# Optimization experiments

Hardware: AMD Instinct MI355X
Metric: run time of the kernel (lower is better)

The kernel has to match this reference:

```python
import jax, jax.numpy as jnp
import numpy as np

B, S, FEAT, H, DK, MAX_ITEMS = 8, 1024, 512, 8, 64, 200
LN_EPS = 1e-5
NEG = -999999999.0


def _build_mask(seq_len):
    # rows before T = S-(maxItems+1) cannot see the tail block [T:];
    # tail rows T..S-2 cannot see columns >= their own index (strict upper wedge).
    T = seq_len - (MAX_ITEMS + 1)
    i = jnp.arange(seq_len)[:, None]
    j = jnp.arange(seq_len)[None, :]
    blocked = ((i < T) & (j >= T)) | ((i >= T) & (i <= seq_len - 2) & (j >= i))
    return jnp.where(blocked, NEG, 0.0).astype(jnp.float32)  # [S, S]


def setup_inputs() -> dict:
    key = jax.random.key(0)
    ks = jax.random.split(key, 6)
    def init(k, shape, fan_in):
        return (jax.random.normal(k, shape, jnp.float32) / np.sqrt(fan_in)).astype(jnp.float32)
    return {
        "x": jax.random.normal(ks[0], (B, S, FEAT), jnp.float32),
        "ln_gamma": jnp.ones((FEAT,), jnp.float32),
        "ln_beta": jnp.zeros((FEAT,), jnp.float32),
        "WQ": init(ks[1], (H, FEAT, DK), FEAT), "bq": jnp.zeros((H, DK), jnp.float32),
        "WK": init(ks[2], (H, FEAT, DK), FEAT), "bk": jnp.zeros((H, DK), jnp.float32),
        "WV": init(ks[3], (H, FEAT, DK), FEAT), "bv": jnp.zeros((H, DK), jnp.float32),
        "WO": init(ks[4], (H * DK, FEAT), H * DK), "bO": jnp.zeros((FEAT,), jnp.float32),
    }


def reference(x, ln_gamma, ln_beta, WQ, bq, WK, bk, WV, bv, WO, bO):
    b, s, f = x.shape
    # Pre-LN
    mu = jnp.mean(x, axis=-1, keepdims=True)
    var = jnp.mean((x - mu) ** 2, axis=-1, keepdims=True)
    xn = (x - mu) / jnp.sqrt(var + LN_EPS) * ln_gamma + ln_beta
    # per-head projections, heads stacked: [B, H, S, DK]
    q = jnp.einsum('bsf,hfd->bhsd', xn, WQ) + bq[None, :, None, :]
    k = jnp.einsum('bsf,hfd->bhsd', xn, WK) + bk[None, :, None, :]
    v = jnp.einsum('bsf,hfd->bhsd', xn, WV) + bv[None, :, None, :]
    scores = jnp.einsum('bhsd,bhtd->bhst', q, k) / np.sqrt(DK).astype(np.float32)
    scores = scores + _build_mask(s)[None, None, :, :]
    attn = jax.nn.softmax(scores, axis=-1)
    z = jnp.einsum('bhst,bhtd->bhsd', attn, v)           # [B, H, S, DK]
    z = jnp.transpose(z, (0, 2, 1, 3)).reshape(b, s, -1)  # concat heads -> [B, S, H*DK]
    return z @ WO + bO
```

## Files before the change

kernel.cpp:

```cpp
#include <hip/hip_runtime.h>

#define S_LEN 1024
#define FEATN 512
#define NH    8
#define DKN   64
#define T_CUT 823
#define LDP   76

typedef __attribute__((ext_vector_type(8))) short v8s;
typedef __attribute__((ext_vector_type(4))) float v4f;
typedef unsigned short u16;

__device__ __forceinline__ float bf2f(u16 u) {
    unsigned v = ((unsigned)u) << 16; float f; __builtin_memcpy(&f, &v, 4); return f;
}
__device__ __forceinline__ u16 f2bf(float f) {
    unsigned v; __builtin_memcpy(&v, &f, 4);
    v += 0x7fffu + ((v >> 16) & 1u);
    return (u16)(v >> 16);
}
__device__ __forceinline__ v4f mfma16(v8s a, v8s b, v4f c) {
    return __builtin_amdgcn_mfma_f32_16x16x32_bf16(a, b, c, 0, 0, 0);
}
__device__ __forceinline__ unsigned cvt_pk_bf16(float a, float b) {
    unsigned r;
    asm("v_cvt_pk_bf16_f32 %0, %1, %2" : "=v"(r) : "v"(a), "v"(b));
    return r;
}

__device__ __forceinline__ int sniff_f32(const void* x) {
    const u16* xs = (const u16*)x;
    int wild = 0;
    #pragma unroll
    for (int i = 0; i < 64; i++) {
        float v = bf2f(xs[i]);
        float a = fabsf(v);
        wild |= (!(a <= 256.f)) | ((v != 0.f) & (a <= 1e-9f));
    }
    return wild;
}

__device__ __forceinline__ float read_in(const void* p, long idx, int fl) {
    return fl ? ((const float*)p)[idx] : bf2f(((const u16*)p)[idx]);
}

__global__ __launch_bounds__(256) void prep_kernel(
    const void* __restrict__ x, const void* __restrict__ lg,
    const void* __restrict__ lb,
    const void* __restrict__ WQ, const void* __restrict__ WK,
    const void* __restrict__ WV, const void* __restrict__ WO,
    u16* __restrict__ xn, u16* __restrict__ BtQKV, u16* __restrict__ BtO)
{
    __shared__ u16 ld[64 * 68];
    const int fl = sniff_f32(x);
    const int b = blockIdx.x, t = threadIdx.x;
    if (b < 192) {
        const int which = b >> 6, rem = b & 63, h = rem >> 3, ktile = rem & 7;
        const void* W = which == 0 ? WQ : (which == 1 ? WK : WV);
        const float sc = (which == 0) ? 0.125f : 1.f;
        #pragma unroll
        for (int i = 0; i < 16; i++) {
            int idx = i * 256 + t, r = idx >> 6, c = idx & 63;
            float v = read_in(W, (long)h * 512 * 64 + (long)(ktile * 64 + r) * 64 + c, fl);
            ld[c * 68 + r] = f2bf(v * sc);
        }
        __syncthreads();
        #pragma unroll
        for (int i = 0; i < 16; i++) {
            int idx = i * 256 + t, d = idx >> 6, kk = idx & 63;
            BtQKV[(long)(which * 512 + h * 64 + d) * 512 + ktile * 64 + kk] = ld[d * 68 + kk];
        }
    } else if (b < 256) {
        const int b2 = b - 192, ntile = b2 >> 3, ktile = b2 & 7;
        #pragma unroll
        for (int i = 0; i < 16; i++) {
            int idx = i * 256 + t, r = idx >> 6, c = idx & 63;
            float v = read_in(WO, (long)(ktile * 64 + r) * 512 + ntile * 64 + c, fl);
            ld[c * 68 + r] = f2bf(v);
        }
        __syncthreads();
        #pragma unroll
        for (int i = 0; i < 16; i++) {
            int idx = i * 256 + t, d = idx >> 6, kk = idx & 63;
            BtO[(long)(ntile * 64 + d) * 512 + ktile * 64 + kk] = ld[d * 68 + kk];
        }
    } else {
        const int w = t >> 6, l = t & 63;
        const int row = (b - 256) * 4 + w;
        float f[8];
        if (fl) {
            const float4* x4 = (const float4*)((const float*)x + (size_t)row * FEATN);
            float4 p0 = x4[l * 2], p1 = x4[l * 2 + 1];
            f[0] = p0.x; f[1] = p0.y; f[2] = p0.z; f[3] = p0.w;
            f[4] = p1.x; f[5] = p1.y; f[6] = p1.z; f[7] = p1.w;
        } else {
            const u16* xu = (const u16*)x + (size_t)row * FEATN + l * 8;
            #pragma unroll
            for (int j = 0; j < 8; j++) f[j] = bf2f(xu[j]);
        }
        float s = 0.f, sq = 0.f;
        #pragma unroll
        for (int j = 0; j < 8; j++) { s += f[j]; sq += f[j] * f[j]; }
        #pragma unroll
        for (int sh = 1; sh < 64; sh <<= 1) { s += __shfl_xor(s, sh); sq += __shfl_xor(sq, sh); }
        const float mu = s * (1.f / 512.f);
        const float var = sq * (1.f / 512.f) - mu * mu;
        const float rstd = rsqrtf(var + 1e-5f);
        u16 o8[8];
        #pragma unroll
        for (int j = 0; j < 8; j++) {
            float gg = read_in(lg, l * 8 + j, fl), bb = read_in(lb, l * 8 + j, fl);
            o8[j] = f2bf((f[j] - mu) * rstd * gg + bb);
        }
        *(v8s*)&xn[(size_t)row * FEATN + l * 8] = *(v8s*)o8;
    }
}

__global__ __launch_bounds__(256) void gemm128(
    const void* __restrict__ x,
    const u16* __restrict__ A, const u16* __restrict__ Bt,
    int N, int K, int mode,
    const void* __restrict__ bq, const void* __restrict__ bk,
    const void* __restrict__ bv,
    u16* __restrict__ qp, u16* __restrict__ kw, u16* __restrict__ vt,
    const void* __restrict__ bO, void* __restrict__ out)
{
    __shared__ __attribute__((aligned(16))) u16 lA[2][128 * 32];
    __shared__ __attribute__((aligned(16))) u16 lB[2][128 * 32];
    const int fl = sniff_f32(x);
    const int bid = blockIdx.x;
    const int xcd = bid & 7, sidx = bid >> 3;
    const int m0 = ((sidx & 7) + xcd * 8) * 128;
    const int n0 = (sidx >> 3) * 128;
    const int t = threadIdx.x;
    const int w = t >> 6, l = t & 63, quad = l >> 4, lr = l & 15;
    const int wr = w >> 1, wc = w & 1;
    v4f acc[4][4] = {};
    const int grow = w * 32 + (l >> 2);
    const int gcol = (l & 3) * 8;
    const u16* Ab = A  + (long)m0 * K;
    const u16* Bb = Bt + (long)n0 * K;

    auto stage = [&](int q, int k0) {
        #pragma unroll
        for (int i = 0; i < 2; i++) {
            __builtin_amdgcn_global_load_lds(
                (const __attribute__((address_space(1))) void*)
                    (Ab + (long)(grow + i * 16) * K + k0 + gcol),
                (__attribute__((address_space(3))) void*)&lA[q][(w * 32 + i * 16) * 32],
                16, 0, 0);
            __builtin_amdgcn_global_load_lds(
                (const __attribute__((address_space(1))) void*)
                    (Bb + (long)(grow + i * 16) * K + k0 + gcol),
                (__attribute__((address_space(3))) void*)&lB[q][(w * 32 + i * 16) * 32],
                16, 0, 0);
        }
    };
    stage(0, 0);
    __syncthreads();
    int cur = 0;
    for (int k0 = 0; k0 < K; k0 += 32) {
        if (k0 + 32 < K) stage(cur ^ 1, k0 + 32);
        v8s af[4], bf[4];
        #pragma unroll
        for (int i = 0; i < 4; i++) {
            af[i] = *(v8s*)&lA[cur][(wr * 64 + i * 16 + lr) * 32 + quad * 8];
            bf[i] = *(v8s*)&lB[cur][(wc * 64 + i * 16 + lr) * 32 + quad * 8];
        }
        #pragma unroll
        for (int i = 0; i < 4; i++)
            #pragma unroll
            for (int j = 0; j < 4; j++)
                acc[i][j] = mfma16(af[i], bf[j], acc[i][j]);
        __syncthreads();
        cur ^= 1;
    }
    #pragma unroll
    for (int i = 0; i < 4; i++)
    #pragma unroll
    for (int j = 0; j < 4; j++) {
        const int mbase = m0 + wr * 64 + i * 16 + quad * 4;
        const int n = n0 + wc * 64 + j * 16 + lr;
        if (mode == 0) {
            const int which = n >> 9, nn = n & 511, h = nn >> 6, d = nn & 63;
            const void* bias = which == 0 ? bq : (which == 1 ? bk : bv);
            const float bs = read_in(bias, nn, fl) * ((which == 0) ? 0.125f : 1.f);
            const int b = mbase >> 10, s = mbase & 1023;
            if (which != 1) {
                u16 v4_[4];
                #pragma unroll
                for (int r = 0; r < 4; r++) v4_[r] = f2bf(acc[i][j][r] + bs);
                u16* dstT = (which == 0) ? qp : vt;
                *(uint2*)&dstT[((size_t)((b * NH + h) * DKN + d)) * S_LEN + s] =
                    *(const uint2*)v4_;
            } else {
                #pragma unroll
                for (int r = 0; r < 4; r++)
                    kw[(((long)(b * NH + h)) * S_LEN + (s + r)) * DKN + d] =
                        f2bf(acc[i][j][r] + bs);
            }
        } else {
            const float bb = read_in(bO, n, fl);
            #pragma unroll
            for (int r = 0; r < 4; r++) {
                float ov = acc[i][j][r] + bb;
                if (fl) ((float*)out)[(long)(mbase + r) * N + n] = ov;
                else    ((u16*)out)[(long)(mbase + r) * N + n] = f2bf(ov);
            }
        }
    }
}

__global__ __launch_bounds__(256) void attn_kernel(
    const u16* __restrict__ qp, const u16* __restrict__ kw,
    const u16* __restrict__ vt, u16* __restrict__ zw)
{
    __shared__ __attribute__((aligned(16))) u16 lk[64 * LDP];
    __shared__ __attribute__((aligned(16))) u16 lv[64 * LDP];
    const int bid = blockIdx.x;
    const int bh = bid & 63, qt = bid >> 6;
    const int q0 = qt * 64, qmax = q0 + 63;
    const int t = threadIdx.x, w = t >> 6, l = t & 63, quad = l >> 4, lr = l & 15;
    const int srow = t >> 2, scg = t & 3;
    const u16* Qp = qp + (size_t)bh * S_LEN * DKN;
    const u16* Kg = kw + (size_t)bh * S_LEN * DKN;
    const u16* Vt = vt + (size_t)bh * S_LEN * DKN;
    v8s aq[2];
    #pragma unroll
    for (int kf = 0; kf < 2; kf++) {
        u16 tmp[8];
        #pragma unroll
        for (int j = 0; j < 8; j++)
            tmp[j] = Qp[(size_t)(kf * 32 + quad * 8 + j) * S_LEN + q0 + w * 16 + lr];
        __builtin_memcpy(&aq[kf], tmp, 16);
    }
    v4f o[4] = {};
    v4f o1 = {};
    v8s vone;
    #pragma unroll
    for (int j = 0; j < 8; j++) vone[j] = (short)0x3f80;
    const int iq = q0 + w * 16 + quad * 4;
    const int i_row = q0 + w * 16 + lr;
    const int jlim = (i_row < T_CUT) ? T_CUT
                   : ((i_row <= S_LEN - 2) ? i_row : 0x40000000);
    const int mx_ = (T_CUT > qmax) ? T_CUT : qmax;
    const int ntiles = (qmax > S_LEN - 2) ? 16 : ((mx_ + 63) >> 6);
    const int vs = 4 * scg;
    v8s kr0 = *(const v8s*)&Kg[srow * DKN + scg * 8];
    v8s kr1 = *(const v8s*)&Kg[srow * DKN + 32 + scg * 8];
    uint2 va0 = *(const uint2*)&Vt[srow * S_LEN + vs];
    uint2 va1 = *(const uint2*)&Vt[srow * S_LEN + 16 + vs];
    uint2 vb0 = *(const uint2*)&Vt[srow * S_LEN + 32 + vs];
    uint2 vb1 = *(const uint2*)&Vt[srow * S_LEN + 48 + vs];

    for (int it = 0; it < ntiles; ++it) {
        const int kt0 = it * 64;
        __syncthreads();
        *(v8s*)&lk[srow * LDP + scg * 8]      = kr0;
        *(v8s*)&lk[srow * LDP + 32 + scg * 8] = kr1;
        {
            unsigned wA[4] = {va0.x, va0.y, va1.x, va1.y};
            unsigned wB[4] = {vb0.x, vb0.y, vb1.x, vb1.y};
            v8s vrA, vrB;
            __builtin_memcpy(&vrA, wA, 16);
            __builtin_memcpy(&vrB, wB, 16);
            *(v8s*)&lv[srow * LDP + scg * 8]      = vrA;
            *(v8s*)&lv[srow * LDP + 32 + scg * 8] = vrB;
        }
        __syncthreads();
        if (it + 1 < ntiles) {
            kr0 = *(const v8s*)&Kg[(kt0 + 64 + srow) * DKN + scg * 8];
            kr1 = *(const v8s*)&Kg[(kt0 + 64 + srow) * DKN + 32 + scg * 8];
            const u16* vrow = &Vt[srow * S_LEN + kt0 + 64];
            va0 = *(const uint2*)(vrow + vs);
            va1 = *(const uint2*)(vrow + 16 + vs);
            vb0 = *(const uint2*)(vrow + 32 + vs);
            vb1 = *(const uint2*)(vrow + 48 + vs);
        }
        v4f sf[4];
        __builtin_amdgcn_s_setprio(1);
        #pragma unroll
        for (int cb = 0; cb < 4; cb++) {
            v8s b0 = *(v8s*)&lk[(cb * 16 + lr) * LDP + quad * 8];
            v8s b1 = *(v8s*)&lk[(cb * 16 + lr) * LDP + 32 + quad * 8];
            v4f z = {};
            z = mfma16(b0, aq[0], z);
            z = mfma16(b1, aq[1], z);
            sf[cb] = z;
        }
        __builtin_amdgcn_s_setprio(0);
        const int kt63 = kt0 + 63;
        const bool tmask = ((q0 < T_CUT) && (kt63 >= T_CUT)) ||
                           ((qmax >= T_CUT) && (kt63 >= q0));
        const int jbase = jlim - kt0 - quad * 4;
        unsigned pu[4][2];
        #pragma unroll
        for (int cb = 0; cb < 4; cb++) {
            float e[4];
            #pragma unroll
            for (int r = 0; r < 4; r++) {
                float ev = __expf(sf[cb][r]);
                if (tmask) ev = (cb * 16 + r >= jbase) ? 0.f : ev;
                e[r] = ev;
            }
            pu[cb][0] = cvt_pk_bf16(e[0], e[1]);
            pu[cb][1] = cvt_pk_bf16(e[2], e[3]);
        }
        v8s ap0, ap1;
        {
            unsigned a0_[4] = {pu[0][0], pu[0][1], pu[1][0], pu[1][1]};
            unsigned a1_[4] = {pu[2][0], pu[2][1], pu[3][0], pu[3][1]};
            __builtin_memcpy(&ap0, a0_, 16);
            __builtin_memcpy(&ap1, a1_, 16);
        }
        __builtin_amdgcn_s_setprio(1);
        #pragma unroll
        for (int db = 0; db < 4; db++) {
            v8s bv0 = *(v8s*)&lv[(db * 16 + lr) * LDP + quad * 8];
            o[db] = mfma16(ap0, bv0, o[db]);
        }
        o1 = mfma16(ap0, vone, o1);
        #pragma unroll
        for (int db = 0; db < 4; db++) {
            v8s bv1 = *(v8s*)&lv[(db * 16 + lr) * LDP + 32 + quad * 8];
            o[db] = mfma16(ap1, bv1, o[db]);
        }
        o1 = mfma16(ap1, vone, o1);
        __builtin_amdgcn_s_setprio(0);
    }
    const int b = bh >> 3, h = bh & 7;
    #pragma unroll
    for (int r = 0; r < 4; r++) {
        const float inv = 1.f / o1[r];
        const int i = iq + r;
        #pragma unroll
        for (int db = 0; db < 4; db++)
            zw[((size_t)b * S_LEN + i) * (NH * DKN) + h * DKN + db * 16 + lr] =
                f2bf(o[db][r] * inv);
    }
}

extern "C" void kernel_launch(void* const* d_in, const int* in_sizes, int n_in,
                              void* d_out, int out_size, void* d_ws, size_t ws_size,
                              hipStream_t stream) {
    const void* x  = d_in[0];
    const void* lg = d_in[1];
    const void* lb = d_in[2];
    const void* WQ = d_in[3];
    const void* bq = d_in[4];
    const void* WK = d_in[5];
    const void* bk = d_in[6];
    const void* WV = d_in[7];
    const void* bv = d_in[8];
    const void* WO = d_in[9];
    const void* bO = d_in[10];

    char* p = (char*)d_ws;
    u16* xn      = (u16*)p;  p += (size_t)8192 * 512 * 2;
    u16* qp      = (u16*)p;  p += (size_t)4194304 * 2;
    u16* kw      = (u16*)p;  p += (size_t)4194304 * 2;
    u16* vt      = (u16*)p;  p += (size_t)4194304 * 2;
    u16* zw      = (u16*)p;  p += (size_t)8192 * 512 * 2;
    u16* BtQKV   = (u16*)p;  p += (size_t)1536 * 512 * 2;
    u16* BtO     = (u16*)p;  p += (size_t)512 * 512 * 2;

    prep_kernel<<<2304, 256, 0, stream>>>(x, lg, lb, WQ, WK, WV, WO, xn, BtQKV, BtO);
    gemm128<<<768, 256, 0, stream>>>(x, xn, BtQKV, 1536, 512, 0,
                                     bq, bk, bv, qp, kw, vt, nullptr, nullptr);
    attn_kernel<<<1024, 256, 0, stream>>>(qp, kw, vt, zw);
    gemm128<<<256, 256, 0, stream>>>(x, zw, BtO, 512, 512, 1,
                                     nullptr, nullptr, nullptr,
                                     nullptr, nullptr, nullptr, bO, d_out);
}
```

Baseline: 176.0 us.

## Process two query sub-tiles per attention block to reuse staged K/V

Each attention block now handles 128 query rows as two 64-row sub-tiles sharing the same LDS-staged K and V tiles, halving the grid to 512 blocks. This halves the global K/V loads and LDS staging per query row, and raises MFMA work per barrier. In exchange it doubles accumulator registers, lowers the number of blocks in flight, and gives up some mask-based skipping at tile granularity.

```diff
diff --git a/kernel.cpp b/kernel.cpp
--- a/kernel.cpp
+++ b/kernel.cpp
@@ -219,30 +219,37 @@
     __shared__ __attribute__((aligned(16))) u16 lv[64 * LDP];
     const int bid = blockIdx.x;
     const int bh = bid & 63, qt = bid >> 6;
-    const int q0 = qt * 64, qmax = q0 + 63;
+    const int q0 = qt * 128, qmax = q0 + 127;
     const int t = threadIdx.x, w = t >> 6, l = t & 63, quad = l >> 4, lr = l & 15;
     const int srow = t >> 2, scg = t & 3;
     const u16* Qp = qp + (size_t)bh * S_LEN * DKN;
     const u16* Kg = kw + (size_t)bh * S_LEN * DKN;
     const u16* Vt = vt + (size_t)bh * S_LEN * DKN;
-    v8s aq[2];
-    #pragma unroll
-    for (int kf = 0; kf < 2; kf++) {
-        u16 tmp[8];
-        #pragma unroll
-        for (int j = 0; j < 8; j++)
-            tmp[j] = Qp[(size_t)(kf * 32 + quad * 8 + j) * S_LEN + q0 + w * 16 + lr];
-        __builtin_memcpy(&aq[kf], tmp, 16);
-    }
-    v4f o[4] = {};
-    v4f o1 = {};
+    v8s aq[2][2];
+    #pragma unroll
+    for (int m = 0; m < 2; m++)
+        #pragma unroll
+        for (int kf = 0; kf < 2; kf++) {
+            u16 tmp[8];
+            #pragma unroll
+            for (int j = 0; j < 8; j++)
+                tmp[j] = Qp[(size_t)(kf * 32 + quad * 8 + j) * S_LEN +
+                            q0 + m * 64 + w * 16 + lr];
+            __builtin_memcpy(&aq[m][kf], tmp, 16);
+        }
+    v4f o[2][4] = {};
+    v4f o1[2] = {};
     v8s vone;
     #pragma unroll
     for (int j = 0; j < 8; j++) vone[j] = (short)0x3f80;
-    const int iq = q0 + w * 16 + quad * 4;
-    const int i_row = q0 + w * 16 + lr;
-    const int jlim = (i_row < T_CUT) ? T_CUT
-                   : ((i_row <= S_LEN - 2) ? i_row : 0x40000000);
+    int iqm[2], jlimm[2];
+    #pragma unroll
+    for (int m = 0; m < 2; m++) {
+        iqm[m] = q0 + m * 64 + w * 16 + quad * 4;
+        const int i_row = q0 + m * 64 + w * 16 + lr;
+        jlimm[m] = (i_row < T_CUT) ? T_CUT
+                 : ((i_row <= S_LEN - 2) ? i_row : 0x40000000);
+    }
     const int mx_ = (T_CUT > qmax) ? T_CUT : qmax;
     const int ntiles = (qmax > S_LEN - 2) ? 16 : ((mx_ + 63) >> 6);
     const int vs = 4 * scg;
@@ -277,66 +284,79 @@
             vb0 = *(const uint2*)(vrow + 32 + vs);
             vb1 = *(const uint2*)(vrow + 48 + vs);
         }
-        v4f sf[4];
+        v4f sf[2][4];
         __builtin_amdgcn_s_setprio(1);
         #pragma unroll
         for (int cb = 0; cb < 4; cb++) {
             v8s b0 = *(v8s*)&lk[(cb * 16 + lr) * LDP + quad * 8];
             v8s b1 = *(v8s*)&lk[(cb * 16 + lr) * LDP + 32 + quad * 8];
-            v4f z = {};
-            z = mfma16(b0, aq[0], z);
-            z = mfma16(b1, aq[1], z);
-            sf[cb] = z;
+            #pragma unroll
+            for (int m = 0; m < 2; m++) {
+                v4f z = {};
+                z = mfma16(b0, aq[m][0], z);
+                z = mfma16(b1, aq[m][1], z);
+                sf[m][cb] = z;
+            }
         }
         __builtin_amdgcn_s_setprio(0);
         const int kt63 = kt0 + 63;
         const bool tmask = ((q0 < T_CUT) && (kt63 >= T_CUT)) ||
                            ((qmax >= T_CUT) && (kt63 >= q0));
-        const int jbase = jlim - kt0 - quad * 4;
-        unsigned pu[4][2];
-        #pragma unroll
-        for (int cb = 0; cb < 4; cb++) {
-            float e[4];
-            #pragma unroll
-            for (int r = 0; r < 4; r++) {
-                float ev = __expf(sf[cb][r]);
-                if (tmask) ev = (cb * 16 + r >= jbase) ? 0.f : ev;
-                e[r] = ev;
+        unsigned pu[2][4][2];
+        #pragma unroll
+        for (int m = 0; m < 2; m++) {
+            const int jbase = jlimm[m] - kt0 - quad * 4;
+            #pragma unroll
+            for (int cb = 0; cb < 4; cb++) {
+                float e[4];
+                #pragma unroll
+                for (int r = 0; r < 4; r++) {
+                    float ev = __expf(sf[m][cb][r]);
+                    if (tmask) ev = (cb * 16 + r >= jbase) ? 0.f : ev;
+                    e[r] = ev;
+                }
+                pu[m][cb][0] = cvt_pk_bf16(e[0], e[1]);
+                pu[m][cb][1] = cvt_pk_bf16(e[2], e[3]);
             }
-            pu[cb][0] = cvt_pk_bf16(e[0], e[1]);
-            pu[cb][1] = cvt_pk_bf16(e[2], e[3]);
-        }
-        v8s ap0, ap1;
-        {
-            unsigned a0_[4] = {pu[0][0], pu[0][1], pu[1][0], pu[1][1]};
-            unsigned a1_[4] = {pu[2][0], pu[2][1], pu[3][0], pu[3][1]};
-            __builtin_memcpy(&ap0, a0_, 16);
-            __builtin_memcpy(&ap1, a1_, 16);
+        }
+        v8s ap[2][2];
+        #pragma unroll
+        for (int m = 0; m < 2; m++) {
+            unsigned a0_[4] = {pu[m][0][0], pu[m][0][1], pu[m][1][0], pu[m][1][1]};
+            unsigned a1_[4] = {pu[m][2][0], pu[m][2][1], pu[m][3][0], pu[m][3][1]};
+            __builtin_memcpy(&ap[m][0], a0_, 16);
+            __builtin_memcpy(&ap[m][1], a1_, 16);
         }
         __builtin_amdgcn_s_setprio(1);
         #pragma unroll
         for (int db = 0; db < 4; db++) {
             v8s bv0 = *(v8s*)&lv[(db * 16 + lr) * LDP + quad * 8];
-            o[db] = mfma16(ap0, bv0, o[db]);
-        }
-        o1 = mfma16(ap0, vone, o1);
+            #pragma unroll
+            for (int m = 0; m < 2; m++) o[m][db] = mfma16(ap[m][0], bv0, o[m][db]);
+        }
+        #pragma unroll
+        for (int m = 0; m < 2; m++) o1[m] = mfma16(ap[m][0], vone, o1[m]);
         #pragma unroll
         for (int db = 0; db < 4; db++) {
             v8s bv1 = *(v8s*)&lv[(db * 16 + lr) * LDP + 32 + quad * 8];
-            o[db] = mfma16(ap1, bv1, o[db]);
-        }
-        o1 = mfma16(ap1, vone, o1);
+            #pragma unroll
+            for (int m = 0; m < 2; m++) o[m][db] = mfma16(ap[m][1], bv1, o[m][db]);
+        }
+        #pragma unroll
+        for (int m = 0; m < 2; m++) o1[m] = mfma16(ap[m][1], vone, o1[m]);
         __builtin_amdgcn_s_setprio(0);
     }
     const int b = bh >> 3, h = bh & 7;
     #pragma unroll
+    for (int m = 0; m < 2; m++)
+    #pragma unroll
     for (int r = 0; r < 4; r++) {
-        const float inv = 1.f / o1[r];
-        const int i = iq + r;
+        const float inv = 1.f / o1[m][r];
+        const int i = iqm[m] + r;
         #pragma unroll
         for (int db = 0; db < 4; db++)
             zw[((size_t)b * S_LEN + i) * (NH * DKN) + h * DKN + db * 16 + lr] =
-                f2bf(o[db][r] * inv);
+                f2bf(o[m][db][r] * inv);
     }
 }
 
@@ -367,7 +387,7 @@
     prep_kernel<<<2304, 256, 0, stream>>>(x, lg, lb, WQ, WK, WV, WO, xn, BtQKV, BtO);
     gemm128<<<768, 256, 0, stream>>>(x, xn, BtQKV, 1536, 512, 0,
                                      bq, bk, bv, qp, kw, vt, nullptr, nullptr);
-    attn_kernel<<<1024, 256, 0, stream>>>(qp, kw, vt, zw);
+    attn_kernel<<<512, 256, 0, stream>>>(qp, kw, vt, zw);
     gemm128<<<256, 256, 0, stream>>>(x, zw, BtO, 512, 512, 1,
                                      nullptr, nullptr, nullptr,
                                      nullptr, nullptr, nullptr, bO, d_out);
```

Result: no change. 176.7 us (+0.4%).

## Double-buffer K/V shared-memory tiles in attention to halve barriers

Applied to the files above, without the earlier changes.

Splits the K and V LDS tiles into two ping-pong buffers. The next tile's global loads are written into the alternate buffer after the current tile's MFMAs, so each iteration needs one barrier instead of two. The aim is to cut per-iteration synchronisation cost and let the LDS writes overlap with compute. In exchange the kernel uses twice the LDS, which may lower occupancy, and the prefetched registers stay live across the compute section.

```diff
diff --git a/kernel.cpp b/kernel.cpp
--- a/kernel.cpp
+++ b/kernel.cpp
@@ -215,8 +215,8 @@
     const u16* __restrict__ qp, const u16* __restrict__ kw,
     const u16* __restrict__ vt, u16* __restrict__ zw)
 {
-    __shared__ __attribute__((aligned(16))) u16 lk[64 * LDP];
-    __shared__ __attribute__((aligned(16))) u16 lv[64 * LDP];
+    __shared__ __attribute__((aligned(16))) u16 lk[2][64 * LDP];
+    __shared__ __attribute__((aligned(16))) u16 lv[2][64 * LDP];
     const int bid = blockIdx.x;
     const int bh = bid & 63, qt = bid >> 6;
     const int q0 = qt * 64, qmax = q0 + 63;
@@ -246,29 +246,31 @@
     const int mx_ = (T_CUT > qmax) ? T_CUT : qmax;
     const int ntiles = (qmax > S_LEN - 2) ? 16 : ((mx_ + 63) >> 6);
     const int vs = 4 * scg;
-    v8s kr0 = *(const v8s*)&Kg[srow * DKN + scg * 8];
-    v8s kr1 = *(const v8s*)&Kg[srow * DKN + 32 + scg * 8];
-    uint2 va0 = *(const uint2*)&Vt[srow * S_LEN + vs];
-    uint2 va1 = *(const uint2*)&Vt[srow * S_LEN + 16 + vs];
-    uint2 vb0 = *(const uint2*)&Vt[srow * S_LEN + 32 + vs];
-    uint2 vb1 = *(const uint2*)&Vt[srow * S_LEN + 48 + vs];
-
+    {
+        v8s kr0 = *(const v8s*)&Kg[srow * DKN + scg * 8];
+        v8s kr1 = *(const v8s*)&Kg[srow * DKN + 32 + scg * 8];
+        uint2 va0 = *(const uint2*)&Vt[srow * S_LEN + vs];
+        uint2 va1 = *(const uint2*)&Vt[srow * S_LEN + 16 + vs];
+        uint2 vb0 = *(const uint2*)&Vt[srow * S_LEN + 32 + vs];
+        uint2 vb1 = *(const uint2*)&Vt[srow * S_LEN + 48 + vs];
+        *(v8s*)&lk[0][srow * LDP + scg * 8]      = kr0;
+        *(v8s*)&lk[0][srow * LDP + 32 + scg * 8] = kr1;
+        unsigned wA[4] = {va0.x, va0.y, va1.x, va1.y};
+        unsigned wB[4] = {vb0.x, vb0.y, vb1.x, vb1.y};
+        v8s vrA, vrB;
+        __builtin_memcpy(&vrA, wA, 16);
+        __builtin_memcpy(&vrB, wB, 16);
+        *(v8s*)&lv[0][srow * LDP + scg * 8]      = vrA;
+        *(v8s*)&lv[0][srow * LDP + 32 + scg * 8] = vrB;
+    }
+    __syncthreads();
+    int cur = 0;
     for (int it = 0; it < ntiles; ++it) {
         const int kt0 = it * 64;
-        __syncthreads();
-        *(v8s*)&lk[srow * LDP + scg * 8]      = kr0;
-        *(v8s*)&lk[srow * LDP + 32 + scg * 8] = kr1;
-        {
-            unsigned wA[4] = {va0.x, va0.y, va1.x, va1.y};
-            unsigned wB[4] = {vb0.x, vb0.y, vb1.x, vb1.y};
-            v8s vrA, vrB;
-            __builtin_memcpy(&vrA, wA, 16);
-            __builtin_memcpy(&vrB, wB, 16);
-            *(v8s*)&lv[srow * LDP + scg * 8]      = vrA;
-            *(v8s*)&lv[srow * LDP + 32 + scg * 8] = vrB;
-        }
-        __syncthreads();
-        if (it + 1 < ntiles) {
+        const bool more = (it + 1 < ntiles);
+        v8s kr0 = {}, kr1 = {};
+        uint2 va0 = {}, va1 = {}, vb0 = {}, vb1 = {};
+        if (more) {
             kr0 = *(const v8s*)&Kg[(kt0 + 64 + srow) * DKN + scg * 8];
             kr1 = *(const v8s*)&Kg[(kt0 + 64 + srow) * DKN + 32 + scg * 8];
             const u16* vrow = &Vt[srow * S_LEN + kt0 + 64];
@@ -281,8 +283,8 @@
         __builtin_amdgcn_s_setprio(1);
         #pragma unroll
         for (int cb = 0; cb < 4; cb++) {
-            v8s b0 = *(v8s*)&lk[(cb * 16 + lr) * LDP + quad * 8];
-            v8s b1 = *(v8s*)&lk[(cb * 16 + lr) * LDP + 32 + quad * 8];
+            v8s b0 = *(v8s*)&lk[cur][(cb * 16 + lr) * LDP + quad * 8];
+            v8s b1 = *(v8s*)&lk[cur][(cb * 16 + lr) * LDP + 32 + quad * 8];
             v4f z = {};
             z = mfma16(b0, aq[0], z);
             z = mfma16(b1, aq[1], z);
@@ -316,17 +318,32 @@
         __builtin_amdgcn_s_setprio(1);
         #pragma unroll
         for (int db = 0; db < 4; db++) {
-            v8s bv0 = *(v8s*)&lv[(db * 16 + lr) * LDP + quad * 8];
+            v8s bv0 = *(v8s*)&lv[cur][(db * 16 + lr) * LDP + quad * 8];
             o[db] = mfma16(ap0, bv0, o[db]);
         }
         o1 = mfma16(ap0, vone, o1);
         #pragma unroll
         for (int db = 0; db < 4; db++) {
-            v8s bv1 = *(v8s*)&lv[(db * 16 + lr) * LDP + 32 + quad * 8];
+            v8s bv1 = *(v8s*)&lv[cur][(db * 16 + lr) * LDP + 32 + quad * 8];
             o[db] = mfma16(ap1, bv1, o[db]);
         }
         o1 = mfma16(ap1, vone, o1);
         __builtin_amdgcn_s_setprio(0);
+        if (more) {
+            *(v8s*)&lk[cur ^ 1][srow * LDP + scg * 8]      = kr0;
+            *(v8s*)&lk[cur ^ 1][srow * LDP + 32 + scg * 8] = kr1;
+            unsigned wA[4] = {va0.x, va0.y, va1.x, va1.y};
+            unsigned wB[4] = {vb0.x, vb0.y, vb1.x, vb1.y};
+            v8s vrA, vrB;
+            __builtin_memcpy(&vrA, wA, 16);
+            __builtin_memcpy(&vrB, wB, 16);
+            *(v8s*)&lv[cur ^ 1][srow * LDP + scg * 8]      = vrA;
+            *(v8s*)&lv[cur ^ 1][srow * LDP + 32 + scg * 8] = vrB;
+        }
+        __asm__ __volatile__("s_waitcnt lgkmcnt(0)" ::: "memory");
+        __builtin_amdgcn_s_barrier();
+        __builtin_amdgcn_sched_barrier(0);
+        cur ^= 1;
     }
     const int b = bh >> 3, h = bh & 7;
     #pragma unroll
```

After: 174.7 us. About the same (-0.8%).
